# Performance work log

Hardware: AMD Instinct MI355X
Metric: run time of the kernel (lower is better)

Reference implementation:

```python
import jax, jax.numpy as jnp
import numpy as np

VARIANCE = (0.1, 0.2)   # SSD variance from init_kwargs
TOP_K = 1000            # max detections / NMS candidates per (image, class)


def _pairwise_iou(b):
    # b: [K,4] in point form (x1,y1,x2,y2)
    area = jnp.maximum(b[:, 2] - b[:, 0], 0.0) * jnp.maximum(b[:, 3] - b[:, 1], 0.0)
    lt = jnp.maximum(b[:, None, :2], b[None, :, :2])
    rb = jnp.minimum(b[:, None, 2:], b[None, :, 2:])
    wh = jnp.maximum(rb - lt, 0.0)
    inter = wh[..., 0] * wh[..., 1]
    union = area[:, None] + area[None, :] - inter
    return inter / jnp.maximum(union, 1e-12)


def _nms_pack(points, csboxes, scores, conf_thresh, nms_thresh):
    # points/csboxes: [P,4]; scores: [P]. Returns [TOP_K, 5] = (score, cx, cy, w, h)
    K = TOP_K
    masked = jnp.where(scores >= conf_thresh, scores, -jnp.inf)
    vals, idx = jax.lax.top_k(masked, K)          # sorted descending
    p = points[idx]                                # [K,4] point form
    cs = csboxes[idx]                              # [K,4] center-size form
    valid = vals >= conf_thresh
    iou = _pairwise_iou(p)                         # [K,K]
    ar = jnp.arange(K)

    def body(i, keep):
        # box i (if kept) suppresses all lower-scored boxes with IoU > thresh
        sup = (iou[i] > nms_thresh) & (ar > i) & keep[i]
        return keep & ~sup

    keep = jax.lax.fori_loop(0, K, body, valid)
    rows = jnp.concatenate([vals[:, None], cs], axis=1)        # [K,5]
    pos = jnp.where(keep, jnp.cumsum(keep) - 1, K)             # compact kept rows to front
    out = jnp.zeros((K, 5), rows.dtype).at[pos].set(rows, mode='drop')
    return out


def setup_inputs() -> dict:
    key = jax.random.key(0)
    k1, k2, k3, k4 = jax.random.split(key, 4)
    B, P, C = 8, 120000, 5
    loc_data = jax.random.normal(k1, (B, 4, P), dtype=jnp.float32) * 0.5
    conf_data = jax.random.normal(k2, (B, C, P), dtype=jnp.float32)
    cxcy = jax.random.uniform(k3, (P, 2), dtype=jnp.float32)
    wh = 0.01 + 0.29 * jax.random.uniform(k4, (P, 2), dtype=jnp.float32)
    prior_data = jnp.concatenate([cxcy, wh], axis=1)           # (cx,cy,w,h) in [0,1]
    return {
        'loc_data': loc_data,
        'conf_data': conf_data,
        'prior_data': prior_data,
        'conf_thresh': jnp.float32(0.05),
        'nms_thresh': jnp.float32(0.5),
    }


def reference(loc_data, conf_data, prior_data, conf_thresh, nms_thresh):
    v0, v1 = VARIANCE
    # softmax over class dim, drop background class 0 -> [B, Cfg, P]
    conf = jax.nn.softmax(conf_data, axis=1)[:, 1:]
    loc = jnp.transpose(loc_data, (0, 2, 1))                   # [B,P,4]
    # SSD decode -> center-size boxes
    cxcy = prior_data[None, :, :2] + loc[..., :2] * v0 * prior_data[None, :, 2:]
    wh = prior_data[None, :, 2:] * jnp.exp(loc[..., 2:] * v1)
    cs = jnp.concatenate([cxcy, wh], axis=-1)                  # [B,P,4] center-size
    pts = jnp.concatenate([cxcy - wh / 2, cxcy + wh / 2], axis=-1)  # [B,P,4] point form
    per_class = jax.vmap(_nms_pack, in_axes=(None, None, 0, None, None))
    per_image = jax.vmap(per_class, in_axes=(0, 0, 0, None, None))
    return per_image(pts, cs, conf, conf_thresh, nms_thresh)   # [B, Cfg, TOP_K, 5]
```

## Files before the change

### kernel.cpp

```cpp
#include <hip/hip_runtime.h>
#include <cstdint>
#include <cstddef>

typedef unsigned long long ull;

#define KTOP   1000
#define CAP    4096
#define HBITS  14
#define HB     (1 << HBITS)
#define HSHIFT (32 - HBITS)
#define ROWS   1024
#define WORDS  16
#define HCHUNK 16
#define GSTAGE 4096

__global__ void decode_kernel(const float* __restrict__ conf,
                              float* __restrict__ scores,
                              unsigned* __restrict__ histz,
                              int histW,
                              int B, int C, int P) {
#pragma clang fp contract(off)
    int t = blockIdx.x * blockDim.x + threadIdx.x;

    for (int i = t; i < histW; i += gridDim.x * blockDim.x) histz[i] = 0u;

    if (t >= B * P) return;
    int b = t / P;
    int p = t - b * P;

    float x[8];
    float m = -INFINITY;
    for (int c = 0; c < C; ++c) {
        x[c] = conf[((size_t)b * C + c) * P + p];
        m = fmaxf(m, x[c]);
    }
    float sum = 0.f;
    for (int c = 0; c < C; ++c) {
        x[c] = expf(x[c] - m);
        sum += x[c];
    }
    for (int c = 1; c < C; ++c) {
        float v = x[c] / sum;
        int bc = b * (C - 1) + (c - 1);
        scores[(size_t)bc * P + p] = v;
    }
}

__global__ void __launch_bounds__(256)
hist_kernel(const float* __restrict__ scores,
            const float* __restrict__ cthp,
            unsigned* __restrict__ hist,
            unsigned* __restrict__ done,
            unsigned* __restrict__ pivot,
            int P) {
    __shared__ unsigned sh[HB / 2];
    __shared__ unsigned T[256];
    __shared__ unsigned s_tk;
    int bc  = blockIdx.x;
    int tid = threadIdx.x;
    float cth = *cthp;

    for (int i = tid; i < HB / 2; i += 256) sh[i] = 0u;
    __syncthreads();

    int chunk = (P + HCHUNK - 1) / HCHUNK;
    int lo = blockIdx.y * chunk;
    int hi = lo + chunk; if (hi > P) hi = P;
    const float* s = scores + (size_t)bc * P;
    for (int p = lo + tid; p < hi; p += 256) {
        float v = s[p];
        if (v >= cth) {
            unsigned bin = __float_as_uint(v) >> HSHIFT;
            atomicAdd(&sh[bin >> 1], (bin & 1u) ? 65536u : 1u);
        }
    }
    __syncthreads();

    unsigned* h = hist + (size_t)bc * HB;
    for (int i = tid; i < HB / 2; i += 256) {
        unsigned v = sh[i];
        if (v & 0xFFFFu)  atomicAdd(&h[2 * i],     v & 0xFFFFu);
        if (v >> 16)      atomicAdd(&h[2 * i + 1], v >> 16);
    }
    __syncthreads();

    if (tid == 0) {
        __threadfence();
        s_tk = __hip_atomic_fetch_add(&done[bc], 1u, __ATOMIC_ACQ_REL, __HIP_MEMORY_SCOPE_AGENT);
    }
    __syncthreads();
    if (s_tk != (unsigned)(gridDim.y - 1)) return;

    const int per = HB / 256;
    int base = tid * per;
    unsigned S = 0;
    for (int i = 0; i < per; ++i)
        S += __hip_atomic_load(&h[base + i], __ATOMIC_RELAXED, __HIP_MEMORY_SCOPE_AGENT);
    T[tid] = S;
    __syncthreads();

    for (int d = 1; d < 256; d <<= 1) {
        unsigned add = (tid + d < 256) ? T[tid + d] : 0u;
        __syncthreads();
        T[tid] += add;
        __syncthreads();
    }

    unsigned Tt = T[tid];
    unsigned Tn = (tid + 1 < 256) ? T[tid + 1] : 0u;
    if (Tt >= (unsigned)KTOP && Tn < (unsigned)KTOP) {
        unsigned cum = Tn;
        for (int i = per - 1; i >= 0; --i) {
            cum += __hip_atomic_load(&h[base + i], __ATOMIC_RELAXED, __HIP_MEMORY_SCOPE_AGENT);
            if (cum >= (unsigned)KTOP) { pivot[bc] = (unsigned)(base + i); break; }
        }
    }
    if (tid == 0 && T[0] < (unsigned)KTOP) pivot[bc] = 0u;
}

__global__ void __launch_bounds__(256)
gather_kernel(const float* __restrict__ scores,
              const unsigned* __restrict__ pivot,
              unsigned* __restrict__ cnt,
              ull* __restrict__ cand,
              const float* __restrict__ cthp, int P) {
    __shared__ ull stage[GSTAGE];
    __shared__ unsigned l_cnt;
    __shared__ unsigned s_base;
    int bc = blockIdx.x;
    const float* s = scores + (size_t)bc * P;
    float cth = *cthp;
    unsigned pv = pivot[bc];
    int nchunk = gridDim.y;
    int chunk = (P + nchunk - 1) / nchunk;
    int lo = blockIdx.y * chunk;
    int hi = lo + chunk; if (hi > P) hi = P;
    int tid  = threadIdx.x;
    int lane = tid & 63;

    if (tid == 0) l_cnt = 0u;
    __syncthreads();

    for (int p0 = lo; p0 < hi; p0 += 256) {
        int p = p0 + tid;
        bool q = false; unsigned k = 0u;
        if (p < hi) {
            float v = s[p];
            k = __float_as_uint(v);
            q = (v >= cth) && ((k >> HSHIFT) >= pv);
        }
        ull mb = __ballot(q);
        if (mb) {
            unsigned wbase = 0u;
            if (lane == 0) wbase = atomicAdd(&l_cnt, (unsigned)__popcll(mb));
            wbase = (unsigned)__shfl((int)wbase, 0);
            if (q) {
                unsigned pos = wbase + (unsigned)__popcll(mb & ((1ull << lane) - 1ull));
                stage[pos] = ((ull)k << 32) | (unsigned)(~(unsigned)p);
            }
        }
    }
    __syncthreads();

    unsigned tot = l_cnt;
    if (tid == 0) s_base = tot ? atomicAdd(&cnt[bc], tot) : 0u;
    __syncthreads();
    unsigned base = s_base;
    ull* cb = cand + (size_t)bc * CAP;
    for (unsigned i = tid; i < tot; i += 256) {
        unsigned off = base + i;
        if (off < CAP) cb[off] = stage[i];
    }
}

__global__ void __launch_bounds__(1024)
sort_kernel(const ull* __restrict__ cand,
            const unsigned* __restrict__ cnt,
            const unsigned* __restrict__ pivot,
            const float* __restrict__ loc,
            const float* __restrict__ prior,
            float* __restrict__ rows,
            float4* __restrict__ pbox,
            float* __restrict__ bar,
            int* __restrict__ nselArr,
            int P, int Cfg) {
#pragma clang fp contract(off)
    int bc  = blockIdx.x;
    int b   = bc / Cfg;
    int tid = threadIdx.x;
    __shared__ ull sbuf[CAP];
    __shared__ unsigned h2[1024];
    __shared__ unsigned s_hi, s_spv, s_m2, s_pos;

    int M = (int)cnt[bc]; if (M > CAP) M = CAP;
    int nsel = M < KTOP ? M : KTOP;
    if (tid == 0) nselArr[bc] = nsel;

    for (int i = tid; i < M; i += 1024)
        sbuf[i] = cand[(size_t)bc * CAP + i];
    __syncthreads();

    int Meff = M;
    if (M > 1024) {
        unsigned pv = pivot[bc];
        h2[tid] = 0u;
        if (tid == 0) { s_hi = 0u; s_pos = 0u; s_spv = 0u; s_m2 = (unsigned)M; }
        __syncthreads();
        for (int i = tid; i < M; i += 1024) {
            unsigned sb32 = (unsigned)(sbuf[i] >> 32);
            if ((sb32 >> HSHIFT) > pv) atomicAdd(&s_hi, 1u);
            else atomicAdd(&h2[(sb32 >> 8) & 1023u], 1u);
        }
        __syncthreads();
        unsigned hicnt = s_hi;
        for (int d = 1; d < 1024; d <<= 1) {
            unsigned add = (tid + d < 1024) ? h2[tid + d] : 0u;
            __syncthreads();
            h2[tid] += add;
            __syncthreads();
        }
        unsigned A  = hicnt + h2[tid];
        unsigned Bv = hicnt + ((tid + 1 < 1024) ? h2[tid + 1] : 0u);
        if (A >= (unsigned)KTOP && Bv < (unsigned)KTOP) { s_spv = (unsigned)tid; s_m2 = A; }
        __syncthreads();
        unsigned thr24 = ((unsigned)pv << 10) | s_spv;
        Meff = (int)s_m2;
        ull my[4];
        #pragma unroll
        for (int j = 0; j < 4; ++j) { int i = tid + (j << 10); my[j] = (i < M) ? sbuf[i] : 0ull; }
        __syncthreads();
        #pragma unroll
        for (int j = 0; j < 4; ++j) {
            int i = tid + (j << 10);
            if (i < M && (unsigned)(my[j] >> 40) >= thr24) {
                unsigned pos = atomicAdd(&s_pos, 1u);
                sbuf[pos] = my[j];
            }
        }
        __syncthreads();
    }

    int n = 1024;
    while (n < Meff) n <<= 1;
    for (int i = tid; i < n; i += 1024)
        if (i >= Meff) sbuf[i] = 0ull;
    __syncthreads();

    for (unsigned k = 2; k <= (unsigned)n; k <<= 1) {
        for (unsigned j = k >> 1; j > 0; j >>= 1) {
            for (unsigned i = tid; i < (unsigned)n; i += 1024) {
                unsigned ixj = i ^ j;
                if (ixj > i) {
                    bool up = ((i & k) == 0u);
                    ull a = sbuf[i], bb = sbuf[ixj];
                    if ((a > bb) == up) { sbuf[i] = bb; sbuf[ixj] = a; }
                }
            }
            __syncthreads();
        }
    }

    for (int r = tid; r < nsel; r += 1024) {
        ull e = sbuf[n - 1 - r];
        float sc = __uint_as_float((unsigned)(e >> 32));
        int idx = (int)(~(unsigned)e);
        float l0 = loc[((size_t)b * 4 + 0) * P + idx];
        float l1 = loc[((size_t)b * 4 + 1) * P + idx];
        float l2 = loc[((size_t)b * 4 + 2) * P + idx];
        float l3 = loc[((size_t)b * 4 + 3) * P + idx];
        float4 pr4 = *(const float4*)(prior + (size_t)idx * 4);
        float cx = pr4.x + (l0 * 0.1f) * pr4.z;
        float cy = pr4.y + (l1 * 0.1f) * pr4.w;
        float w  = pr4.z * expf(l2 * 0.2f);
        float h  = pr4.w * expf(l3 * 0.2f);
        float x1 = cx - w / 2.f, y1 = cy - h / 2.f;
        float x2 = cx + w / 2.f, y2 = cy + h / 2.f;
        size_t sb = (size_t)bc * ROWS + r;
        pbox[sb] = make_float4(x1, y1, x2, y2);
        bar[sb]  = fmaxf(x2 - x1, 0.f) * fmaxf(y2 - y1, 0.f);
        float* rr = rows + ((size_t)bc * KTOP + r) * 5;
        rr[0] = sc; rr[1] = cx; rr[2] = cy; rr[3] = w; rr[4] = h;
    }
}

__global__ void __launch_bounds__(1024)
mask_kernel(const float4* __restrict__ pbox,
            const float* __restrict__ bar,
            const int* __restrict__ nselArr,
            const float* __restrict__ nthp,
            ull* __restrict__ mask) {
#pragma clang fp contract(off)
    int bc   = blockIdx.x;
    int tile = blockIdx.y;
    int tid  = threadIdx.x;
    int nsel = nselArr[bc];
    float nth = *nthp;

    __shared__ float4 sbox[ROWS];
    __shared__ float  sar[ROWS];
    size_t sb = (size_t)bc * ROWS;
    sbox[tid] = pbox[sb + tid];
    sar[tid]  = bar[sb + tid];
    __syncthreads();

    int wv   = tid >> 6;
    int lane = tid & 63;
    int i0   = tile * 64 + (wv << 2);

    ull rowbits[4] = {0ull, 0ull, 0ull, 0ull};
    if (i0 < nsel) {
        float4 bi[4]; float ai[4];
        #pragma unroll
        for (int r = 0; r < 4; ++r) { bi[r] = sbox[i0 + r]; ai[r] = sar[i0 + r]; }

        int whi = (nsel + 63) >> 6; if (whi > WORDS) whi = WORDS;
        for (int w = tile; w < whi; ++w) {
            int j = (w << 6) + lane;
            float4 bj = sbox[j];
            float  aj = sar[j];
            #pragma unroll
            for (int r = 0; r < 4; ++r) {
                int i = i0 + r;
                float ww = fmaxf(fminf(bi[r].z, bj.z) - fmaxf(bi[r].x, bj.x), 0.f);
                float hh = fmaxf(fminf(bi[r].w, bj.w) - fmaxf(bi[r].y, bj.y), 0.f);
                float inter = ww * hh;
                float uni = ai[r] + aj - inter;
                float iou = inter / fmaxf(uni, 1e-12f);
                bool ok = (j > i) && (j < nsel) && (iou > nth);
                ull bits = __ballot(ok);
                if (lane == w) rowbits[r] = bits;
            }
        }
    }
    #pragma unroll
    for (int r = 0; r < 4; ++r)
        if (lane < WORDS)
            mask[(((size_t)bc * ROWS + (i0 + r)) << 4) + lane] = rowbits[r];
}

__device__ __forceinline__ void nms_chunk_body(
    int c, int nchunk, int lane, int g, int w,
    const ull* __restrict__ mrow, ull* sm,
    ull (&pr)[16], ull (&st)[16], ull& S)
{
    int cb = (c & 1) << 10;
    int nb = ((c + 1) & 1) << 10;
    if (c + 2 < nchunk) {
        #pragma unroll
        for (int k = 0; k < 16; ++k)
            pr[k] = mrow[(size_t)(c + 2) * 1024 + k * 64 + lane];
    }

    ull cur = __shfl(S, c);
    ull dbuf[16], dnxt[16];
    #pragma unroll
    for (int k = 0; k < 16; ++k) dbuf[k] = sm[cb + (k << 4) + c];
    #pragma unroll
    for (int grp = 0; grp < 4; ++grp) {
        if (grp < 3) {
            #pragma unroll
            for (int k = 0; k < 16; ++k)
                dnxt[k] = sm[cb + ((((grp + 1) << 4) + k) << 4) + c];
        }
        #pragma unroll
        for (int k = 0; k < 16; ++k) {
            int i = (grp << 4) + k;
            ull supm = (ull)((long long)(cur << (63 - i)) >> 63);
            cur |= dbuf[k] & ~supm;
        }
        if (grp < 3) {
            #pragma unroll
            for (int k = 0; k < 16; ++k) dbuf[k] = dnxt[k];
        }
    }
    ull kbits = ~cur;

    unsigned sub = (unsigned)((kbits >> (g << 4)) & 0xFFFFull);
    int rbase2 = cb + (g << 8) + w;
    ull part = 0ull;
    #pragma unroll
    for (int i = 0; i < 16; ++i) {
        ull v = sm[rbase2 + (i << 4)];
        part |= v & (ull)(0ll - (long long)((sub >> i) & 1u));
    }
    part |= __shfl_xor(part, 16);
    part |= __shfl_xor(part, 32);
    S |= part;
    if (lane == c) S = cur;

    if (c + 1 < nchunk) {
        #pragma unroll
        for (int k = 0; k < 16; ++k) sm[nb + k * 64 + lane] = st[k];
    }
}

__global__ void __launch_bounds__(256)
reduce_pack_kernel(const ull* __restrict__ mask,
                   const int* __restrict__ nselArr,
                   const float* __restrict__ rows,
                   float* __restrict__ out) {
    int bc  = blockIdx.x;
    int tid = threadIdx.x;
    int nsel = nselArr[bc];
    const ull* mrow = mask + ((size_t)bc * ROWS << 4);

    __shared__ ull sm[2048];
    __shared__ ull kw[WORDS];
    __shared__ unsigned pref[WORDS + 1];

    if (tid < 64) {
        int lane = tid;
        int nchunk = (nsel + 63) >> 6;
        ull S = 0ull;
        int g = lane >> 4;
        int w = lane & 15;

        ull ra[16], rb[16];
        if (nchunk > 0) {
            #pragma unroll
            for (int k = 0; k < 16; ++k) ra[k] = mrow[k * 64 + lane];
            if (nchunk > 1) {
                #pragma unroll
                for (int k = 0; k < 16; ++k) rb[k] = mrow[1024 + k * 64 + lane];
            }
            #pragma unroll
            for (int k = 0; k < 16; ++k) sm[k * 64 + lane] = ra[k];

            #pragma unroll 1
            for (int cc = 0; cc < 8; ++cc) {
                int c0 = cc << 1;
                if (c0 >= nchunk) break;
                nms_chunk_body(c0, nchunk, lane, g, w, mrow, sm, ra, rb, S);
                int c1 = c0 + 1;
                if (c1 >= nchunk) break;
                nms_chunk_body(c1, nchunk, lane, g, w, mrow, sm, rb, ra, S);
            }
        }

        if (lane < WORDS) {
            int base_i = lane << 6;
            ull valid = 0ull;
            int rem = nsel - base_i;
            if (rem > 0) valid = (rem >= 64) ? ~0ull : ((1ull << rem) - 1ull);
            kw[lane] = (~S) & valid;
        }
    }
    __syncthreads();

    if (tid == 0) {
        unsigned c = 0;
        for (int w = 0; w < WORDS; ++w) { pref[w] = c; c += (unsigned)__popcll(kw[w]); }
        pref[WORDS] = c;
    }
    __syncthreads();
    unsigned tot = pref[WORDS];

    const float* rbase = rows + (size_t)bc * KTOP * 5;
    float* obase = out + (size_t)bc * KTOP * 5;
    for (int r = tid; r < KTOP; r += 256) {
        ull wv = kw[r >> 6];
        if ((wv >> (r & 63)) & 1ull) {
            int pos = (int)pref[r >> 6] + __popcll(wv & ((1ull << (r & 63)) - 1ull));
            const float* rr = rbase + r * 5;
            float* oo = obase + pos * 5;
            oo[0] = rr[0]; oo[1] = rr[1]; oo[2] = rr[2]; oo[3] = rr[3]; oo[4] = rr[4];
        }
        if (r >= (int)tot) {
            float* oo = obase + r * 5;
            oo[0] = 0.f; oo[1] = 0.f; oo[2] = 0.f; oo[3] = 0.f; oo[4] = 0.f;
        }
    }
}

extern "C" void kernel_launch(void* const* d_in, const int* in_sizes, int n_in,
                              void* d_out, int out_size, void* d_ws, size_t ws_size,
                              hipStream_t stream) {
    (void)n_in; (void)out_size; (void)ws_size;
    const float* loc   = (const float*)d_in[0];
    const float* conf  = (const float*)d_in[1];
    const float* prior = (const float*)d_in[2];
    const float* cth   = (const float*)d_in[3];
    const float* nth   = (const float*)d_in[4];
    float* out = (float*)d_out;

    int P   = in_sizes[2] / 4;
    int B   = in_sizes[0] / (4 * P);
    int C   = in_sizes[1] / (B * P);
    int Cfg = C - 1;
    int NBC = B * Cfg;

    char* base = (char*)d_ws;
    size_t off = 0;
    auto carve = [&](size_t bytes) { char* p = base + off; off = (off + bytes + 255) & ~(size_t)255; return p; };

    float4*   pbox   = (float4*)  carve((size_t)NBC * ROWS * 16);
    ull*      cand   = (ull*)     carve((size_t)NBC * CAP * 8);
    ull*      mask   = (ull*)     carve((size_t)NBC * ROWS * WORDS * 8);
    float*    scores = (float*)   carve((size_t)NBC * P * 4);
    float*    rows   = (float*)   carve((size_t)NBC * KTOP * 5 * 4);
    float*    bar    = (float*)   carve((size_t)NBC * ROWS * 4);
    unsigned* hist   = (unsigned*)carve((size_t)NBC * HB * 4 + (size_t)2 * NBC * 4);
    unsigned* cnt    = hist + (size_t)NBC * HB;
    unsigned* done   = cnt + NBC;
    unsigned* pivot  = (unsigned*)carve((size_t)NBC * 4);
    int*      nselA  = (int*)     carve((size_t)NBC * 4);

    int histW = NBC * HB + 2 * NBC;

    int GY = (P + GSTAGE - 1) / GSTAGE;
    if (GY < 32) GY = 32;

    int n1 = B * P;
    decode_kernel<<<(n1 + 255) / 256, 256, 0, stream>>>(conf, scores, hist, histW, B, C, P);
    hist_kernel<<<dim3(NBC, HCHUNK), 256, 0, stream>>>(scores, cth, hist, done, pivot, P);
    gather_kernel<<<dim3(NBC, GY), 256, 0, stream>>>(scores, pivot, cnt, cand, cth, P);
    sort_kernel<<<NBC, 1024, 0, stream>>>(cand, cnt, pivot, loc, prior, rows, pbox, bar, nselA, P, Cfg);
    mask_kernel<<<dim3(NBC, ROWS / 64), 1024, 0, stream>>>(pbox, bar, nselA, nth, mask);
    reduce_pack_kernel<<<NBC, 256, 0, stream>>>(mask, nselA, rows, out);
}
```

Baseline: 220.8 us.

## Shrink score histogram to 512 upper bins and compute pivot inside gather blocks

The histogram covers only the top 512 of the 16K float-bit bins above a fixed offset, and everything below is clamped into bin zero. The last-block-done atomic counter and its pivot scan are removed; each gather block now rebuilds the pivot from the small histogram with a shared-memory prefix scan. Histogram chunking grows from 16 to 64 blocks per class. This cuts histogram zeroing, flush atomics and the serialized tail scan, but every gather block repeats the scan, and the fixed bin offset assumes scores fall in a known float range.

```diff
diff --git a/kernel.cpp b/kernel.cpp
--- a/kernel.cpp
+++ b/kernel.cpp
@@ -7,11 +7,12 @@
 #define KTOP   1000
 #define CAP    4096
 #define HBITS  14
-#define HB     (1 << HBITS)
 #define HSHIFT (32 - HBITS)
+#define NB2    512
+#define BLO    3584
 #define ROWS   1024
 #define WORDS  16
-#define HCHUNK 16
+#define HCHUNK 64
 #define GSTAGE 4096
 
 __global__ void decode_kernel(const float* __restrict__ conf,
@@ -50,96 +51,77 @@
 hist_kernel(const float* __restrict__ scores,
             const float* __restrict__ cthp,
             unsigned* __restrict__ hist,
-            unsigned* __restrict__ done,
-            unsigned* __restrict__ pivot,
             int P) {
-    __shared__ unsigned sh[HB / 2];
-    __shared__ unsigned T[256];
-    __shared__ unsigned s_tk;
+    __shared__ unsigned sh[NB2 / 2];
     int bc  = blockIdx.x;
     int tid = threadIdx.x;
     float cth = *cthp;
 
-    for (int i = tid; i < HB / 2; i += 256) sh[i] = 0u;
-    __syncthreads();
-
-    int chunk = (P + HCHUNK - 1) / HCHUNK;
+    sh[tid] = 0u;
+    __syncthreads();
+
+    int chunk = (P + gridDim.y - 1) / gridDim.y;
     int lo = blockIdx.y * chunk;
     int hi = lo + chunk; if (hi > P) hi = P;
     const float* s = scores + (size_t)bc * P;
     for (int p = lo + tid; p < hi; p += 256) {
         float v = s[p];
         if (v >= cth) {
-            unsigned bin = __float_as_uint(v) >> HSHIFT;
-            atomicAdd(&sh[bin >> 1], (bin & 1u) ? 65536u : 1u);
-        }
-    }
-    __syncthreads();
-
-    unsigned* h = hist + (size_t)bc * HB;
-    for (int i = tid; i < HB / 2; i += 256) {
-        unsigned v = sh[i];
-        if (v & 0xFFFFu)  atomicAdd(&h[2 * i],     v & 0xFFFFu);
-        if (v >> 16)      atomicAdd(&h[2 * i + 1], v >> 16);
-    }
-    __syncthreads();
-
-    if (tid == 0) {
-        __threadfence();
-        s_tk = __hip_atomic_fetch_add(&done[bc], 1u, __ATOMIC_ACQ_REL, __HIP_MEMORY_SCOPE_AGENT);
-    }
-    __syncthreads();
-    if (s_tk != (unsigned)(gridDim.y - 1)) return;
-
-    const int per = HB / 256;
-    int base = tid * per;
-    unsigned S = 0;
-    for (int i = 0; i < per; ++i)
-        S += __hip_atomic_load(&h[base + i], __ATOMIC_RELAXED, __HIP_MEMORY_SCOPE_AGENT);
-    T[tid] = S;
-    __syncthreads();
-
-    for (int d = 1; d < 256; d <<= 1) {
-        unsigned add = (tid + d < 256) ? T[tid + d] : 0u;
-        __syncthreads();
-        T[tid] += add;
-        __syncthreads();
-    }
-
-    unsigned Tt = T[tid];
-    unsigned Tn = (tid + 1 < 256) ? T[tid + 1] : 0u;
-    if (Tt >= (unsigned)KTOP && Tn < (unsigned)KTOP) {
-        unsigned cum = Tn;
-        for (int i = per - 1; i >= 0; --i) {
-            cum += __hip_atomic_load(&h[base + i], __ATOMIC_RELAXED, __HIP_MEMORY_SCOPE_AGENT);
-            if (cum >= (unsigned)KTOP) { pivot[bc] = (unsigned)(base + i); break; }
-        }
-    }
-    if (tid == 0 && T[0] < (unsigned)KTOP) pivot[bc] = 0u;
+            int bl = (int)(__float_as_uint(v) >> HSHIFT) - BLO;
+            if (bl < 0) bl = 0;
+            atomicAdd(&sh[bl >> 1], (bl & 1) ? 65536u : 1u);
+        }
+    }
+    __syncthreads();
+
+    unsigned* h = hist + (size_t)bc * NB2;
+    unsigned v = sh[tid];
+    if (v & 0xFFFFu)  atomicAdd(&h[2 * tid],     v & 0xFFFFu);
+    if (v >> 16)      atomicAdd(&h[2 * tid + 1], v >> 16);
 }
 
 __global__ void __launch_bounds__(256)
 gather_kernel(const float* __restrict__ scores,
-              const unsigned* __restrict__ pivot,
+              const unsigned* __restrict__ hist,
+              unsigned* __restrict__ pivot,
               unsigned* __restrict__ cnt,
               ull* __restrict__ cand,
               const float* __restrict__ cthp, int P) {
     __shared__ ull stage[GSTAGE];
-    __shared__ unsigned l_cnt;
-    __shared__ unsigned s_base;
+    __shared__ unsigned T[256];
+    __shared__ unsigned s_pv, l_cnt, s_base;
     int bc = blockIdx.x;
+    int tid  = threadIdx.x;
+    int lane = tid & 63;
     const float* s = scores + (size_t)bc * P;
     float cth = *cthp;
-    unsigned pv = pivot[bc];
+
+    const unsigned* h = hist + (size_t)bc * NB2;
+    unsigned s0 = h[2 * tid], s1 = h[2 * tid + 1];
+    T[tid] = s0 + s1;
+    if (tid == 0) { s_pv = 0u; l_cnt = 0u; }
+    __syncthreads();
+    for (int d = 1; d < 256; d <<= 1) {
+        unsigned add = (tid + d < 256) ? T[tid + d] : 0u;
+        __syncthreads();
+        T[tid] += add;
+        __syncthreads();
+    }
+    unsigned Tt = T[tid];
+    unsigned Tn = (tid + 1 < 256) ? T[tid + 1] : 0u;
+    if (Tt >= (unsigned)KTOP && Tn < (unsigned)KTOP) {
+        unsigned pl = (Tn + s1 >= (unsigned)KTOP) ? (2u * tid + 1u) : (2u * tid);
+        s_pv = pl + (unsigned)BLO;
+    }
+    __syncthreads();
+    unsigned pv = s_pv;
+    if (pv <= (unsigned)BLO) pv = 0u;
+    if (blockIdx.y == 0 && tid == 0) pivot[bc] = pv;
+
     int nchunk = gridDim.y;
     int chunk = (P + nchunk - 1) / nchunk;
     int lo = blockIdx.y * chunk;
     int hi = lo + chunk; if (hi > P) hi = P;
-    int tid  = threadIdx.x;
-    int lane = tid & 63;
-
-    if (tid == 0) l_cnt = 0u;
-    __syncthreads();
 
     for (int p0 = lo; p0 < hi; p0 += 256) {
         int p = p0 + tid;
@@ -499,21 +481,20 @@
     float*    scores = (float*)   carve((size_t)NBC * P * 4);
     float*    rows   = (float*)   carve((size_t)NBC * KTOP * 5 * 4);
     float*    bar    = (float*)   carve((size_t)NBC * ROWS * 4);
-    unsigned* hist   = (unsigned*)carve((size_t)NBC * HB * 4 + (size_t)2 * NBC * 4);
-    unsigned* cnt    = hist + (size_t)NBC * HB;
-    unsigned* done   = cnt + NBC;
+    unsigned* hist   = (unsigned*)carve((size_t)NBC * NB2 * 4 + (size_t)NBC * 4);
+    unsigned* cnt    = hist + (size_t)NBC * NB2;
     unsigned* pivot  = (unsigned*)carve((size_t)NBC * 4);
     int*      nselA  = (int*)     carve((size_t)NBC * 4);
 
-    int histW = NBC * HB + 2 * NBC;
+    int histW = NBC * NB2 + NBC;
 
     int GY = (P + GSTAGE - 1) / GSTAGE;
     if (GY < 32) GY = 32;
 
     int n1 = B * P;
     decode_kernel<<<(n1 + 255) / 256, 256, 0, stream>>>(conf, scores, hist, histW, B, C, P);
-    hist_kernel<<<dim3(NBC, HCHUNK), 256, 0, stream>>>(scores, cth, hist, done, pivot, P);
-    gather_kernel<<<dim3(NBC, GY), 256, 0, stream>>>(scores, pivot, cnt, cand, cth, P);
+    hist_kernel<<<dim3(NBC, HCHUNK), 256, 0, stream>>>(scores, cth, hist, P);
+    gather_kernel<<<dim3(NBC, GY), 256, 0, stream>>>(scores, hist, pivot, cnt, cand, cth, P);
     sort_kernel<<<NBC, 1024, 0, stream>>>(cand, cnt, pivot, loc, prior, rows, pbox, bar, nselA, P, Cfg);
     mask_kernel<<<dim3(NBC, ROWS / 64), 1024, 0, stream>>>(pbox, bar, nselA, nth, mask);
     reduce_pack_kernel<<<NBC, 256, 0, stream>>>(mask, nselA, rows, out);
```

After: 183.8 us. 1.2x faster.
